# Optimization experiments

Measured on AMD Instinct MI355X. Metric: run time of the kernel, lower is better.

The kernel has to match this reference:

```python
import jax, jax.numpy as jnp
import numpy as np

N_NODES = 50000
N_EDGES = 800000
D_IN, D_HID, D_OUT = 128, 128, 64


def setup_inputs() -> dict:
    key = jax.random.key(0)
    ks = jax.random.split(key, 8)
    x = jax.random.normal(ks[0], (N_NODES, D_IN), dtype=jnp.float32)
    edge_index = jax.random.randint(ks[1], (2, N_EDGES), 0, N_NODES, dtype=jnp.int64)
    s1 = 1.0 / np.sqrt(D_IN)
    s2 = 1.0 / np.sqrt(D_HID)
    # PyG SAGEConv: out = lin_l(mean_aggr(x_j)) + lin_r(x_root); bias lives in lin_l
    Wl1 = jax.random.uniform(ks[2], (D_HID, D_IN), jnp.float32, -s1, s1)
    bl1 = jnp.zeros((D_HID,), jnp.float32)
    Wr1 = jax.random.uniform(ks[3], (D_HID, D_IN), jnp.float32, -s1, s1)
    Wl2 = jax.random.uniform(ks[4], (D_OUT, D_HID), jnp.float32, -s2, s2)
    bl2 = jnp.zeros((D_OUT,), jnp.float32)
    Wr2 = jax.random.uniform(ks[5], (D_OUT, D_HID), jnp.float32, -s2, s2)
    return {"x": x, "edge_index": edge_index, "Wl1": Wl1, "bl1": bl1, "Wr1": Wr1,
            "Wl2": Wl2, "bl2": bl2, "Wr2": Wr2}


def _sage_conv(x, src, dst, Wl, bl, Wr):
    # mean aggregation of source-node features onto destination nodes
    msg = x[src]                                              # [E, d]
    agg = jax.ops.segment_sum(msg, dst, num_segments=N_NODES)  # [N, d]
    cnt = jax.ops.segment_sum(jnp.ones((src.shape[0],), x.dtype), dst,
                              num_segments=N_NODES)            # [N]
    mean = agg / jnp.maximum(cnt, 1.0)[:, None]
    return mean @ Wl.T + bl + x @ Wr.T


def reference(x, edge_index, Wl1, bl1, Wr1, Wl2, bl2, Wr2):
    src, dst = edge_index[0], edge_index[1]
    h = jax.nn.relu(_sage_conv(x, src, dst, Wl1, bl1, Wr1))
    h = jax.nn.relu(_sage_conv(h, src, dst, Wl2, bl2, Wr2))
    return jax.nn.log_softmax(h, axis=-1)
```

## Files before the change

kernel.cpp:

```cpp
#include <hip/hip_runtime.h>
#include <cstdint>
#include <cstddef>

#define N_NODES 50000
#define N_EDGES 800000
#define ROWS_PAD 50048
#define ZROW 50000
#define BUCKET_CAP 64

#define CNT_POISON 0xAAAAAAAAu
__device__ __forceinline__ unsigned cnt_decode(unsigned raw) {
  return raw > 0x40000000u ? raw - CNT_POISON : raw;
}

typedef _Float16 f16;
typedef _Float16 f16x8 __attribute__((ext_vector_type(8)));
typedef float f32x2 __attribute__((ext_vector_type(2)));
typedef float f32x4 __attribute__((ext_vector_type(4)));
typedef float fx4 __attribute__((ext_vector_type(4)));
typedef unsigned int u32x2 __attribute__((ext_vector_type(2)));
typedef unsigned short us4 __attribute__((ext_vector_type(4)));


#define NRANGE 8
#define NCHUNK 200
#define CHUNK_E (N_EDGES / NCHUNK)
#define NB_FILL (NCHUNK * NRANGE)
#define NB_CX 3125
#define NB_CW 192
#define RANGE_SZ (N_NODES / NRANGE)

__global__ __launch_bounds__(256) void preprocess_kernel(
    const int* __restrict__ edge, unsigned* __restrict__ cnt, unsigned short* __restrict__ bucket,
    const float* __restrict__ x, f16* __restrict__ X16, unsigned char* __restrict__ X8,
    unsigned char* __restrict__ Hp8,
    const float* __restrict__ Wl1, const float* __restrict__ Wr1,
    const float* __restrict__ Wl2, const float* __restrict__ Wr2,
    f16* __restrict__ Wc1, f16* __restrict__ Wc2p) {
  const int b = blockIdx.x;
  const int tid = threadIdx.x;
  if (b < NB_FILL) {
    const int cg = b >> 6, r = (b >> 3) & 7, cl = b & 7;
    const int chunk = cg * 8 + cl;
    const int lo = r * RANGE_SZ, hi = lo + RANGE_SZ;
    const int e0 = chunk * CHUNK_E;
    #pragma unroll
    for (int i = 0; i < 16; ++i) {
      const int e = e0 + tid + i * 256;
      if (e < e0 + CHUNK_E) {
        const int dst = edge[N_EDGES + e];
        if (dst >= lo && dst < hi) {
          const int src = edge[e];
          const unsigned pos = cnt_decode(atomicAdd(&cnt[dst], 1u));
          if (pos < BUCKET_CAP) bucket[(size_t)dst * BUCKET_CAP + pos] = (unsigned short)src;
        }
      }
    }
  } else if (b < NB_FILL + NB_CX) {
    const int idx = (b - NB_FILL) * 256 + tid;
    const int row = idx >> 4, c8 = idx & 15;
    const fx4 v0 = __builtin_nontemporal_load(
        reinterpret_cast<const fx4*>(x + (size_t)row * 128 + c8 * 8));
    const fx4 v1 = __builtin_nontemporal_load(
        reinterpret_cast<const fx4*>(x + (size_t)row * 128 + c8 * 8 + 4));
    f16x8 o;
    o[0] = (f16)v0[0]; o[1] = (f16)v0[1]; o[2] = (f16)v0[2]; o[3] = (f16)v0[3];
    o[4] = (f16)v1[0]; o[5] = (f16)v1[1]; o[6] = (f16)v1[2]; o[7] = (f16)v1[3];
    *reinterpret_cast<f16x8*>(X16 + (size_t)row * 128 + c8 * 8) = o;
    u32x2 p;
    int w = __builtin_amdgcn_cvt_pk_fp8_f32(v0[0], v0[1], 0, false);
    w = __builtin_amdgcn_cvt_pk_fp8_f32(v0[2], v0[3], w, true);
    p[0] = (unsigned int)w;
    w = __builtin_amdgcn_cvt_pk_fp8_f32(v1[0], v1[1], 0, false);
    w = __builtin_amdgcn_cvt_pk_fp8_f32(v1[2], v1[3], w, true);
    p[1] = (unsigned int)w;
    *reinterpret_cast<u32x2*>(X8 + (size_t)row * 128 + c8 * 8) = p;
  } else if (b < NB_FILL + NB_CX + NB_CW) {
    const int idx = (b - NB_FILL - NB_CX) * 256 + tid;
    if (idx < 128 * 256) {
      const int n = idx >> 8, k = idx & 255;
      Wc1[idx] = (f16)((k < 128) ? Wl1[n * 128 + k] : Wr1[n * 128 + (k - 128)]);
    } else {
      const int j = idx - 128 * 256;
      const int n = j >> 7, k = j & 127;
      Wc2p[j] = (f16)((n < 64) ? Wl2[n * 128 + k] : Wr2[(n - 64) * 128 + k]);
    }
  } else {
    if (tid < 32)
      reinterpret_cast<unsigned int*>(X8 + (size_t)ZROW * 128)[tid] = 0u;
    else if (tid < 48)
      reinterpret_cast<unsigned int*>(Hp8 + (size_t)ZROW * 64)[tid - 32] = 0u;
  }
}


__device__ __forceinline__ void aggregate_to_lds(
    const unsigned char* __restrict__ F8, const unsigned* __restrict__ cnt,
    const unsigned short* __restrict__ bucket,
    f16 (*M)[136], int wid, int lane) {
  const int quad = lane >> 4, l16 = lane & 15;
  const int nb0 = blockIdx.x * 32 + wid * 8;
  const int dv = (lane < 8) ? (int)cnt_decode(cnt[nb0 + lane]) : 0;
  us4 b4g[2];
  #pragma unroll
  for (int g = 0; g < 2; ++g)
    b4g[g] = __builtin_nontemporal_load(reinterpret_cast<const us4*>(
        bucket + (size_t)(nb0 + g * 4 + quad) * BUCKET_CAP + l16 * 4));
  const unsigned char* Fsrc = F8 + l16 * 8;
  #pragma unroll 1
  for (int g = 0; g < 2; ++g) {
    const int dq = __shfl(dv, g * 4 + quad, 64);
    const int dqc = min(dq, BUCKET_CAP);
    int md = max(max(__shfl(dv, g * 4 + 0, 64), __shfl(dv, g * 4 + 1, 64)),
                 max(__shfl(dv, g * 4 + 2, 64), __shfl(dv, g * 4 + 3, 64)));
    md = min(md, BUCKET_CAP);
    const us4 b4 = b4g[g];
    float acc[8];
    #pragma unroll
    for (int c = 0; c < 8; ++c) acc[c] = 0.f;
    for (int j = 0; j < md; j += 16) {
      u32x2 v[16];
      #pragma unroll
      for (int k = 0; k < 16; ++k) {
        const int slot = j + k;
        const int idx = __shfl((int)b4[k & 3], quad * 16 + (slot >> 2), 64);
        const int row = (slot < dqc) ? idx : ZROW;
        v[k] = *reinterpret_cast<const u32x2*>(Fsrc + (size_t)row * 128);
      }
      #pragma unroll
      for (int k = 0; k < 16; ++k) {
        const f32x2 f0 = __builtin_amdgcn_cvt_pk_f32_fp8((int)v[k][0], false);
        const f32x2 f1 = __builtin_amdgcn_cvt_pk_f32_fp8((int)v[k][0], true);
        const f32x2 f2 = __builtin_amdgcn_cvt_pk_f32_fp8((int)v[k][1], false);
        const f32x2 f3 = __builtin_amdgcn_cvt_pk_f32_fp8((int)v[k][1], true);
        acc[0] += f0[0]; acc[1] += f0[1]; acc[2] += f1[0]; acc[3] += f1[1];
        acc[4] += f2[0]; acc[5] += f2[1]; acc[6] += f3[0]; acc[7] += f3[1];
      }
    }
    const float inv = 1.0f / (float)(dq > 0 ? dq : 1);
    f16x8 o;
    #pragma unroll
    for (int c = 0; c < 8; ++c) o[c] = (f16)(acc[c] * inv);
    *reinterpret_cast<f16x8*>(&M[wid * 8 + g * 4 + quad][l16 * 8]) = o;
  }
}


__global__ __launch_bounds__(256, 4) void layer1_kernel(
    const f16* __restrict__ X16, const unsigned char* __restrict__ X8,
    const unsigned* __restrict__ cnt, const unsigned short* __restrict__ bucket,
    const f16* __restrict__ Wc, const float* __restrict__ bias,
    const f16* __restrict__ Wc2p,
    unsigned char* __restrict__ Hp8, f16* __restrict__ R2f) {
  __shared__ f16 M[32][136];
  __shared__ f16 HT[32][136];
  const int wid = threadIdx.x >> 6, lane = threadIdx.x & 63;
  const int quad = lane >> 4, l16 = lane & 15;
  const int rhalf = wid & 1, nhalf = wid >> 1;
  const int row0 = blockIdx.x * 32 + rhalf * 16;
  const f16* Xrow = X16 + (size_t)(row0 + l16) * 128 + quad * 8;
  f16x8 rr[4];
  #pragma unroll
  for (int s2 = 0; s2 < 4; ++s2)
    rr[s2] = __builtin_nontemporal_load(reinterpret_cast<const f16x8*>(Xrow + s2 * 32));
  aggregate_to_lds(X8, cnt, bucket, M, wid, lane);
  __syncthreads();
  f32x4 acc[4];
  #pragma unroll
  for (int t = 0; t < 4; ++t) acc[t] = (f32x4){0.f, 0.f, 0.f, 0.f};
  const f16x8* Wb = reinterpret_cast<const f16x8*>(Wc) + quad;
  #pragma unroll
  for (int s = 0; s < 8; ++s) {
    const f16x8 a = (s < 4)
        ? *reinterpret_cast<const f16x8*>(&M[rhalf * 16 + l16][quad * 8 + s * 32])
        : rr[s - 4];
    #pragma unroll
    for (int t = 0; t < 4; ++t) {
      const int u = nhalf * 4 + t;
      const f16x8 bb = Wb[(u * 16 + l16) * 32 + s * 4];
      acc[t] = __builtin_amdgcn_mfma_f32_16x16x32_f16(a, bb, acc[t], 0, 0, 0);
    }
  }
  #pragma unroll
  for (int t = 0; t < 4; ++t) {
    const int col = (nhalf * 4 + t) * 16 + l16;
    const float bv = bias[col];
    #pragma unroll
    for (int r = 0; r < 4; ++r) {
      const int rl = rhalf * 16 + quad * 4 + r;
      HT[rl][col] = (f16)fmaxf(acc[t][r] + bv, 0.f);
    }
  }
  __syncthreads();
  f32x4 acc2[4];
  #pragma unroll
  for (int t = 0; t < 4; ++t) acc2[t] = (f32x4){0.f, 0.f, 0.f, 0.f};
  const f16x8* Wb2 = reinterpret_cast<const f16x8*>(Wc2p) + quad;
  #pragma unroll
  for (int s = 0; s < 4; ++s) {
    const f16x8 a2 = *reinterpret_cast<const f16x8*>(&HT[rhalf * 16 + l16][quad * 8 + s * 32]);
    #pragma unroll
    for (int t = 0; t < 4; ++t) {
      const int u = nhalf * 4 + t;
      const f16x8 bb = Wb2[(u * 16 + l16) * 16 + s * 4];
      acc2[t] = __builtin_amdgcn_mfma_f32_16x16x32_f16(a2, bb, acc2[t], 0, 0, 0);
    }
  }
  #pragma unroll
  for (int t = 0; t < 4; ++t) {
    const int u = nhalf * 4 + t;
    const int col2 = u * 16 + l16;
    #pragma unroll
    for (int r = 0; r < 4; ++r) {
      const int row = row0 + quad * 4 + r;
      if (row < N_NODES) {
        const float vv = acc2[t][r];
        if (u < 4) {
          const int p = __builtin_amdgcn_cvt_pk_fp8_f32(vv, vv, 0, false);
          Hp8[(size_t)row * 64 + col2] = (unsigned char)(p & 0xFF);
        } else {
          R2f[(size_t)row * 64 + (col2 - 64)] = (f16)vv;
        }
      }
    }
  }
}


__global__ __launch_bounds__(256, 4) void layer2_kernel(
    const unsigned char* __restrict__ Hp8, const f16* __restrict__ R2f,
    const unsigned* __restrict__ cnt, const unsigned short* __restrict__ bucket,
    const float* __restrict__ bias, float* __restrict__ out) {
  __shared__ f16 M2[32][72];
  const int wid = threadIdx.x >> 6, lane = threadIdx.x & 63;
  const int quad = lane >> 4, l16 = lane & 15;
  const int half8 = l16 >> 3, l8 = l16 & 7;
  const int nb0 = blockIdx.x * 32 + wid * 8;
  const int dv = (lane < 8) ? (int)cnt_decode(cnt[nb0 + lane]) : 0;
  us4 b4g[2];
  #pragma unroll
  for (int g = 0; g < 2; ++g)
    b4g[g] = __builtin_nontemporal_load(reinterpret_cast<const us4*>(
        bucket + (size_t)(nb0 + g * 4 + quad) * BUCKET_CAP + l16 * 4));
  const unsigned char* Fsrc = Hp8 + l8 * 8;
  #pragma unroll 1
  for (int g = 0; g < 2; ++g) {
    const int dq = __shfl(dv, g * 4 + quad, 64);
    const int dqc = min(dq, BUCKET_CAP);
    int md = max(max(__shfl(dv, g * 4 + 0, 64), __shfl(dv, g * 4 + 1, 64)),
                 max(__shfl(dv, g * 4 + 2, 64), __shfl(dv, g * 4 + 3, 64)));
    md = min(md, BUCKET_CAP);
    const us4 b4 = b4g[g];
    float acc[8];
    #pragma unroll
    for (int c = 0; c < 8; ++c) acc[c] = 0.f;
    for (int j = 0; j < md; j += 32) {
      u32x2 v[16];
      #pragma unroll
      for (int k = 0; k < 16; ++k) {
        const int slot = j + k + half8 * 16;
        const int idx = __shfl((int)b4[k & 3],
                               quad * 16 + ((j + k) >> 2) + half8 * 4, 64);
        const int row = (slot < dqc) ? idx : ZROW;
        v[k] = *reinterpret_cast<const u32x2*>(Fsrc + (size_t)row * 64);
      }
      #pragma unroll
      for (int k = 0; k < 16; ++k) {
        const f32x2 f0 = __builtin_amdgcn_cvt_pk_f32_fp8((int)v[k][0], false);
        const f32x2 f1 = __builtin_amdgcn_cvt_pk_f32_fp8((int)v[k][0], true);
        const f32x2 f2 = __builtin_amdgcn_cvt_pk_f32_fp8((int)v[k][1], false);
        const f32x2 f3 = __builtin_amdgcn_cvt_pk_f32_fp8((int)v[k][1], true);
        acc[0] += f0[0]; acc[1] += f0[1]; acc[2] += f1[0]; acc[3] += f1[1];
        acc[4] += f2[0]; acc[5] += f2[1]; acc[6] += f3[0]; acc[7] += f3[1];
      }
    }
    #pragma unroll
    for (int c = 0; c < 8; ++c) acc[c] += __shfl_xor(acc[c], 8, 64);
    const float inv = 1.0f / (float)(dq > 0 ? dq : 1);
    f16x8 o;
    #pragma unroll
    for (int c = 0; c < 8; ++c) o[c] = (f16)(acc[c] * inv);
    *reinterpret_cast<f16x8*>(&M2[wid * 8 + g * 4 + quad][l8 * 8]) = o;
  }
  __syncthreads();
  const int rl = wid * 8 + (lane >> 3);
  const int row = blockIdx.x * 32 + rl;
  const f16x8 mv = *reinterpret_cast<const f16x8*>(&M2[rl][l8 * 8]);
  f16x8 r2v = {};
  if (row < N_NODES)
    r2v = *reinterpret_cast<const f16x8*>(R2f + (size_t)row * 64 + l8 * 8);
  const fx4 b0 = *reinterpret_cast<const fx4*>(bias + l8 * 8);
  const fx4 b1 = *reinterpret_cast<const fx4*>(bias + l8 * 8 + 4);
  float v[8];
  #pragma unroll
  for (int c = 0; c < 8; ++c) {
    const float bb = (c < 4) ? b0[c] : b1[c - 4];
    v[c] = fmaxf((float)mv[c] + (float)r2v[c] + bb, 0.f);
  }
  float m = v[0];
  #pragma unroll
  for (int c = 1; c < 8; ++c) m = fmaxf(m, v[c]);
  #pragma unroll
  for (int off = 1; off < 8; off <<= 1) m = fmaxf(m, __shfl_xor(m, off, 64));
  float s = 0.f;
  #pragma unroll
  for (int c = 0; c < 8; ++c) s += __expf(v[c] - m);
  #pragma unroll
  for (int off = 1; off < 8; off <<= 1) s += __shfl_xor(s, off, 64);
  const float ls = m + __logf(s);
  if (row < N_NODES) {
    fx4 o0, o1;
    #pragma unroll
    for (int c = 0; c < 4; ++c) { o0[c] = v[c] - ls; o1[c] = v[c + 4] - ls; }
    __builtin_nontemporal_store(o0, reinterpret_cast<fx4*>(out + (size_t)row * 64 + l8 * 8));
    __builtin_nontemporal_store(o1, reinterpret_cast<fx4*>(out + (size_t)row * 64 + l8 * 8 + 4));
  }
}


extern "C" void kernel_launch(void* const* d_in, const int* in_sizes, int n_in,
                              void* d_out, int out_size, void* d_ws, size_t ws_size,
                              hipStream_t stream) {
  const float* x   = (const float*)d_in[0];
  const int* edge  = (const int*)d_in[1];
  const float* Wl1 = (const float*)d_in[2];
  const float* bl1 = (const float*)d_in[3];
  const float* Wr1 = (const float*)d_in[4];
  const float* Wl2 = (const float*)d_in[5];
  const float* bl2 = (const float*)d_in[6];
  const float* Wr2 = (const float*)d_in[7];
  float* out = (float*)d_out;

  char* ws = (char*)d_ws;
  size_t off = 0;
  auto alloc = [&](size_t bytes) -> char* {
    char* p = ws + off;
    off = (off + bytes + 255) & ~(size_t)255;
    return p;
  };
  unsigned* cnt          = (unsigned*)alloc((size_t)ROWS_PAD * 4);
  unsigned short* bucket = (unsigned short*)alloc((size_t)ROWS_PAD * BUCKET_CAP * 2);
  f16* X16           = (f16*)alloc((size_t)ROWS_PAD * 128 * 2);
  unsigned char* X8  = (unsigned char*)alloc((size_t)ROWS_PAD * 128);
  unsigned char* Hp8 = (unsigned char*)alloc((size_t)ROWS_PAD * 64);
  f16* R2f           = (f16*)alloc((size_t)ROWS_PAD * 64 * 2);
  f16* Wc1           = (f16*)alloc((size_t)128 * 256 * 2);
  f16* Wc2p          = (f16*)alloc((size_t)128 * 128 * 2);


  preprocess_kernel<<<NB_FILL + NB_CX + NB_CW + 1, 256, 0, stream>>>(
      edge, cnt, bucket, x, X16, X8, Hp8, Wl1, Wr1, Wl2, Wr2, Wc1, Wc2p);

  layer1_kernel<<<ROWS_PAD / 32, 256, 0, stream>>>(
      X16, X8, cnt, bucket, Wc1, bl1, Wc2p, Hp8, R2f);
  layer2_kernel<<<ROWS_PAD / 32, 256, 0, stream>>>(
      Hp8, R2f, cnt, bucket, bl2, out);
}
```

Before: 198.7 us.

## Apply layer-1 linear transform before aggregation and fold it into preprocessing

Layer 1 now computes x@Wl1^T and x@Wr1^T inside the preprocess kernel, using MFMA on fp32 inputs converted to fp16 on the fly, and stores the projected features in fp8 and the root term in fp16. The layer-1 kernel then only gathers and averages the pre-projected rows, adds the root term and bias, and applies relu before going straight into the layer-2 GEMM. This removes the separate x conversion pass, the Wc1 packing, and the first GEMM stage that sat after aggregation. In exchange the preprocess kernel does a GEMM that now runs alongside the edge bucketing. Rounding the projected features to fp8 instead of the raw inputs changes numerical error.

```diff
diff --git a/kernel.cpp b/kernel.cpp
--- a/kernel.cpp
+++ b/kernel.cpp
@@ -26,17 +26,17 @@
 #define NCHUNK 200
 #define CHUNK_E (N_EDGES / NCHUNK)
 #define NB_FILL (NCHUNK * NRANGE)
-#define NB_CX 3125
-#define NB_CW 192
+#define NB_GEMM (ROWS_PAD / 32)
+#define NB_W 64
 #define RANGE_SZ (N_NODES / NRANGE)
 
 __global__ __launch_bounds__(256) void preprocess_kernel(
     const int* __restrict__ edge, unsigned* __restrict__ cnt, unsigned short* __restrict__ bucket,
-    const float* __restrict__ x, f16* __restrict__ X16, unsigned char* __restrict__ X8,
-    unsigned char* __restrict__ Hp8,
+    const float* __restrict__ x,
     const float* __restrict__ Wl1, const float* __restrict__ Wr1,
     const float* __restrict__ Wl2, const float* __restrict__ Wr2,
-    f16* __restrict__ Wc1, f16* __restrict__ Wc2p) {
+    unsigned char* __restrict__ Xp8, f16* __restrict__ Xrf,
+    unsigned char* __restrict__ Hp8, f16* __restrict__ Wc2p) {
   const int b = blockIdx.x;
   const int tid = threadIdx.x;
   if (b < NB_FILL) {
@@ -56,47 +56,84 @@
         }
       }
     }
-  } else if (b < NB_FILL + NB_CX) {
-    const int idx = (b - NB_FILL) * 256 + tid;
-    const int row = idx >> 4, c8 = idx & 15;
-    const fx4 v0 = __builtin_nontemporal_load(
-        reinterpret_cast<const fx4*>(x + (size_t)row * 128 + c8 * 8));
-    const fx4 v1 = __builtin_nontemporal_load(
-        reinterpret_cast<const fx4*>(x + (size_t)row * 128 + c8 * 8 + 4));
-    f16x8 o;
-    o[0] = (f16)v0[0]; o[1] = (f16)v0[1]; o[2] = (f16)v0[2]; o[3] = (f16)v0[3];
-    o[4] = (f16)v1[0]; o[5] = (f16)v1[1]; o[6] = (f16)v1[2]; o[7] = (f16)v1[3];
-    *reinterpret_cast<f16x8*>(X16 + (size_t)row * 128 + c8 * 8) = o;
-    u32x2 p;
-    int w = __builtin_amdgcn_cvt_pk_fp8_f32(v0[0], v0[1], 0, false);
-    w = __builtin_amdgcn_cvt_pk_fp8_f32(v0[2], v0[3], w, true);
-    p[0] = (unsigned int)w;
-    w = __builtin_amdgcn_cvt_pk_fp8_f32(v1[0], v1[1], 0, false);
-    w = __builtin_amdgcn_cvt_pk_fp8_f32(v1[2], v1[3], w, true);
-    p[1] = (unsigned int)w;
-    *reinterpret_cast<u32x2*>(X8 + (size_t)row * 128 + c8 * 8) = p;
-  } else if (b < NB_FILL + NB_CX + NB_CW) {
-    const int idx = (b - NB_FILL - NB_CX) * 256 + tid;
-    if (idx < 128 * 256) {
-      const int n = idx >> 8, k = idx & 255;
-      Wc1[idx] = (f16)((k < 128) ? Wl1[n * 128 + k] : Wr1[n * 128 + (k - 128)]);
-    } else {
-      const int j = idx - 128 * 256;
-      const int n = j >> 7, k = j & 127;
-      Wc2p[j] = (f16)((n < 64) ? Wl2[n * 128 + k] : Wr2[(n - 64) * 128 + k]);
-    }
+  } else if (b < NB_FILL + NB_GEMM) {
+    const int tile = b - NB_FILL;
+    const int wid = tid >> 6, lane = tid & 63;
+    const int quad = lane >> 4, l16 = lane & 15;
+    const int rhalf = wid & 1, nhalf = wid >> 1;
+    const int rowA = tile * 32 + rhalf * 16 + l16;
+    const bool aok = rowA < N_NODES;
+    const float* xrow = x + (size_t)rowA * 128;
+    f16x8 a[4];
+    #pragma unroll
+    for (int s = 0; s < 4; ++s) {
+      const int k0 = quad * 8 + s * 32;
+      fx4 u0 = {0.f, 0.f, 0.f, 0.f}, u1 = {0.f, 0.f, 0.f, 0.f};
+      if (aok) {
+        u0 = *reinterpret_cast<const fx4*>(xrow + k0);
+        u1 = *reinterpret_cast<const fx4*>(xrow + k0 + 4);
+      }
+      f16x8 av;
+      av[0] = (f16)u0[0]; av[1] = (f16)u0[1]; av[2] = (f16)u0[2]; av[3] = (f16)u0[3];
+      av[4] = (f16)u1[0]; av[5] = (f16)u1[1]; av[6] = (f16)u1[2]; av[7] = (f16)u1[3];
+      a[s] = av;
+    }
+    const int row0c = tile * 32 + rhalf * 16;
+    #pragma unroll 1
+    for (int m = 0; m < 2; ++m) {
+      const float* W = m ? Wr1 : Wl1;
+      f32x4 acc[4];
+      #pragma unroll
+      for (int t = 0; t < 4; ++t) acc[t] = (f32x4){0.f, 0.f, 0.f, 0.f};
+      #pragma unroll
+      for (int s = 0; s < 4; ++s) {
+        #pragma unroll
+        for (int t = 0; t < 4; ++t) {
+          const int n = (nhalf * 4 + t) * 16 + l16;
+          const int k0 = (s * 4 + quad) * 8;
+          const fx4 w0 = *reinterpret_cast<const fx4*>(W + n * 128 + k0);
+          const fx4 w1 = *reinterpret_cast<const fx4*>(W + n * 128 + k0 + 4);
+          f16x8 bb;
+          bb[0] = (f16)w0[0]; bb[1] = (f16)w0[1]; bb[2] = (f16)w0[2]; bb[3] = (f16)w0[3];
+          bb[4] = (f16)w1[0]; bb[5] = (f16)w1[1]; bb[6] = (f16)w1[2]; bb[7] = (f16)w1[3];
+          acc[t] = __builtin_amdgcn_mfma_f32_16x16x32_f16(a[s], bb, acc[t], 0, 0, 0);
+        }
+      }
+      #pragma unroll
+      for (int t = 0; t < 4; ++t) {
+        const int col = (nhalf * 4 + t) * 16 + l16;
+        #pragma unroll
+        for (int r = 0; r < 4; ++r) {
+          const int rowg = row0c + quad * 4 + r;
+          if (rowg < N_NODES) {
+            const float vv = acc[t][r];
+            if (m == 0) {
+              const int p = __builtin_amdgcn_cvt_pk_fp8_f32(vv, vv, 0, false);
+              Xp8[(size_t)rowg * 128 + col] = (unsigned char)(p & 0xFF);
+            } else {
+              Xrf[(size_t)rowg * 128 + col] = (f16)vv;
+            }
+          }
+        }
+      }
+    }
+  } else if (b < NB_FILL + NB_GEMM + NB_W) {
+    const int idx = (b - NB_FILL - NB_GEMM) * 256 + tid;
+    const int n = idx >> 7, k = idx & 127;
+    Wc2p[idx] = (f16)((n < 64) ? Wl2[n * 128 + k] : Wr2[(n - 64) * 128 + k]);
   } else {
     if (tid < 32)
-      reinterpret_cast<unsigned int*>(X8 + (size_t)ZROW * 128)[tid] = 0u;
+      reinterpret_cast<unsigned int*>(Xp8 + (size_t)ZROW * 128)[tid] = 0u;
     else if (tid < 48)
       reinterpret_cast<unsigned int*>(Hp8 + (size_t)ZROW * 64)[tid - 32] = 0u;
   }
 }
 
 
-__device__ __forceinline__ void aggregate_to_lds(
-    const unsigned char* __restrict__ F8, const unsigned* __restrict__ cnt,
-    const unsigned short* __restrict__ bucket,
+__device__ __forceinline__ void aggregate_fused(
+    const unsigned char* __restrict__ Xp8, const f16* __restrict__ Xrf,
+    const float* __restrict__ bias,
+    const unsigned* __restrict__ cnt, const unsigned short* __restrict__ bucket,
     f16 (*M)[136], int wid, int lane) {
   const int quad = lane >> 4, l16 = lane & 15;
   const int nb0 = blockIdx.x * 32 + wid * 8;
@@ -106,7 +143,9 @@
   for (int g = 0; g < 2; ++g)
     b4g[g] = __builtin_nontemporal_load(reinterpret_cast<const us4*>(
         bucket + (size_t)(nb0 + g * 4 + quad) * BUCKET_CAP + l16 * 4));
-  const unsigned char* Fsrc = F8 + l16 * 8;
+  const unsigned char* Fsrc = Xp8 + l16 * 8;
+  const fx4 bc0 = *reinterpret_cast<const fx4*>(bias + l16 * 8);
+  const fx4 bc1 = *reinterpret_cast<const fx4*>(bias + l16 * 8 + 4);
   #pragma unroll 1
   for (int g = 0; g < 2; ++g) {
     const int dq = __shfl(dv, g * 4 + quad, 64);
@@ -138,59 +177,30 @@
       }
     }
     const float inv = 1.0f / (float)(dq > 0 ? dq : 1);
+    const f16x8 xr = *reinterpret_cast<const f16x8*>(
+        Xrf + (size_t)(nb0 + g * 4 + quad) * 128 + l16 * 8);
     f16x8 o;
     #pragma unroll
-    for (int c = 0; c < 8; ++c) o[c] = (f16)(acc[c] * inv);
+    for (int c = 0; c < 8; ++c) {
+      const float bb = (c < 4) ? bc0[c] : bc1[c - 4];
+      o[c] = (f16)fmaxf(acc[c] * inv + (float)xr[c] + bb, 0.f);
+    }
     *reinterpret_cast<f16x8*>(&M[wid * 8 + g * 4 + quad][l16 * 8]) = o;
   }
 }
 
 
 __global__ __launch_bounds__(256, 4) void layer1_kernel(
-    const f16* __restrict__ X16, const unsigned char* __restrict__ X8,
+    const unsigned char* __restrict__ Xp8, const f16* __restrict__ Xrf,
     const unsigned* __restrict__ cnt, const unsigned short* __restrict__ bucket,
-    const f16* __restrict__ Wc, const float* __restrict__ bias,
-    const f16* __restrict__ Wc2p,
+    const float* __restrict__ bias, const f16* __restrict__ Wc2p,
     unsigned char* __restrict__ Hp8, f16* __restrict__ R2f) {
   __shared__ f16 M[32][136];
-  __shared__ f16 HT[32][136];
   const int wid = threadIdx.x >> 6, lane = threadIdx.x & 63;
   const int quad = lane >> 4, l16 = lane & 15;
   const int rhalf = wid & 1, nhalf = wid >> 1;
   const int row0 = blockIdx.x * 32 + rhalf * 16;
-  const f16* Xrow = X16 + (size_t)(row0 + l16) * 128 + quad * 8;
-  f16x8 rr[4];
-  #pragma unroll
-  for (int s2 = 0; s2 < 4; ++s2)
-    rr[s2] = __builtin_nontemporal_load(reinterpret_cast<const f16x8*>(Xrow + s2 * 32));
-  aggregate_to_lds(X8, cnt, bucket, M, wid, lane);
-  __syncthreads();
-  f32x4 acc[4];
-  #pragma unroll
-  for (int t = 0; t < 4; ++t) acc[t] = (f32x4){0.f, 0.f, 0.f, 0.f};
-  const f16x8* Wb = reinterpret_cast<const f16x8*>(Wc) + quad;
-  #pragma unroll
-  for (int s = 0; s < 8; ++s) {
-    const f16x8 a = (s < 4)
-        ? *reinterpret_cast<const f16x8*>(&M[rhalf * 16 + l16][quad * 8 + s * 32])
-        : rr[s - 4];
-    #pragma unroll
-    for (int t = 0; t < 4; ++t) {
-      const int u = nhalf * 4 + t;
-      const f16x8 bb = Wb[(u * 16 + l16) * 32 + s * 4];
-      acc[t] = __builtin_amdgcn_mfma_f32_16x16x32_f16(a, bb, acc[t], 0, 0, 0);
-    }
-  }
-  #pragma unroll
-  for (int t = 0; t < 4; ++t) {
-    const int col = (nhalf * 4 + t) * 16 + l16;
-    const float bv = bias[col];
-    #pragma unroll
-    for (int r = 0; r < 4; ++r) {
-      const int rl = rhalf * 16 + quad * 4 + r;
-      HT[rl][col] = (f16)fmaxf(acc[t][r] + bv, 0.f);
-    }
-  }
+  aggregate_fused(Xp8, Xrf, bias, cnt, bucket, M, wid, lane);
   __syncthreads();
   f32x4 acc2[4];
   #pragma unroll
@@ -198,7 +208,7 @@
   const f16x8* Wb2 = reinterpret_cast<const f16x8*>(Wc2p) + quad;
   #pragma unroll
   for (int s = 0; s < 4; ++s) {
-    const f16x8 a2 = *reinterpret_cast<const f16x8*>(&HT[rhalf * 16 + l16][quad * 8 + s * 32]);
+    const f16x8 a2 = *reinterpret_cast<const f16x8*>(&M[rhalf * 16 + l16][quad * 8 + s * 32]);
     #pragma unroll
     for (int t = 0; t < 4; ++t) {
       const int u = nhalf * 4 + t;
@@ -340,19 +350,18 @@
   };
   unsigned* cnt          = (unsigned*)alloc((size_t)ROWS_PAD * 4);
   unsigned short* bucket = (unsigned short*)alloc((size_t)ROWS_PAD * BUCKET_CAP * 2);
-  f16* X16           = (f16*)alloc((size_t)ROWS_PAD * 128 * 2);
-  unsigned char* X8  = (unsigned char*)alloc((size_t)ROWS_PAD * 128);
+  unsigned char* Xp8 = (unsigned char*)alloc((size_t)ROWS_PAD * 128);
+  f16* Xrf           = (f16*)alloc((size_t)ROWS_PAD * 128 * 2);
   unsigned char* Hp8 = (unsigned char*)alloc((size_t)ROWS_PAD * 64);
   f16* R2f           = (f16*)alloc((size_t)ROWS_PAD * 64 * 2);
-  f16* Wc1           = (f16*)alloc((size_t)128 * 256 * 2);
   f16* Wc2p          = (f16*)alloc((size_t)128 * 128 * 2);
 
 
-  preprocess_kernel<<<NB_FILL + NB_CX + NB_CW + 1, 256, 0, stream>>>(
-      edge, cnt, bucket, x, X16, X8, Hp8, Wl1, Wr1, Wl2, Wr2, Wc1, Wc2p);
+  preprocess_kernel<<<NB_FILL + NB_GEMM + NB_W + 1, 256, 0, stream>>>(
+      edge, cnt, bucket, x, Wl1, Wr1, Wl2, Wr2, Xp8, Xrf, Hp8, Wc2p);
 
   layer1_kernel<<<ROWS_PAD / 32, 256, 0, stream>>>(
-      X16, X8, cnt, bucket, Wc1, bl1, Wc2p, Hp8, R2f);
+      Xp8, Xrf, cnt, bucket, bl1, Wc2p, Hp8, R2f);
   layer2_kernel<<<ROWS_PAD / 32, 256, 0, stream>>>(
       Hp8, R2f, cnt, bucket, bl2, out);
 }
```

Result: slower. 222.2 us (+11.9%).
